# Kernel optimization log

Hardware: AMD Instinct MI355X
Metric: run time of the kernel (lower is better)

The kernel has to match this reference:

```python
import jax, jax.numpy as jnp
import numpy as np

N = 50000      # nodes
E = 800000     # edges (before self-loops)
IN = 128       # input_dim
HID = 64       # hidden_dim
EMB = 32       # embedding_dim
HEADS = 4
NEG_SLOPE = 0.2
BN_EPS = 1e-5


def setup_inputs() -> dict:
    key = jax.random.key(0)
    ks = jax.random.split(key, 20)
    s = 0.1
    x = jax.random.normal(ks[0], (N, IN), jnp.float32)
    edge_index = jax.random.randint(ks[1], (2, E), 0, N, dtype=jnp.int64)
    # GAT layer 0: 128 -> 64, 4 heads, concat
    W0 = jax.random.normal(ks[2], (IN, HEADS * HID), jnp.float32) * s
    a_src0 = jax.random.normal(ks[3], (HEADS, HID), jnp.float32) * s
    a_dst0 = jax.random.normal(ks[4], (HEADS, HID), jnp.float32) * s
    b0 = jax.random.normal(ks[5], (HEADS * HID,), jnp.float32) * s
    # BatchNorm1d(256) in eval mode (running stats)
    bn_gamma = jax.random.uniform(ks[6], (HEADS * HID,), jnp.float32, 0.5, 1.5)
    bn_beta = jax.random.normal(ks[7], (HEADS * HID,), jnp.float32) * s
    bn_mean = jax.random.normal(ks[8], (HEADS * HID,), jnp.float32) * s
    bn_var = jax.random.uniform(ks[9], (HEADS * HID,), jnp.float32, 0.5, 1.5)
    # GAT layer 1: 256 -> 32, 1 head, mean (concat=False)
    W1 = jax.random.normal(ks[10], (HEADS * HID, EMB), jnp.float32) * s
    a_src1 = jax.random.normal(ks[11], (1, EMB), jnp.float32) * s
    a_dst1 = jax.random.normal(ks[12], (1, EMB), jnp.float32) * s
    b1 = jax.random.normal(ks[13], (EMB,), jnp.float32) * s
    # prediction head: Linear(32,64) -> ReLU -> Linear(64,1)
    head_W1 = jax.random.normal(ks[14], (EMB, HID), jnp.float32) * s
    head_b1 = jax.random.normal(ks[15], (HID,), jnp.float32) * s
    head_W2 = jax.random.normal(ks[16], (HID, 1), jnp.float32) * s
    head_b2 = jax.random.normal(ks[17], (1,), jnp.float32) * s
    return dict(x=x, edge_index=edge_index, W0=W0, a_src0=a_src0, a_dst0=a_dst0, b0=b0,
                bn_gamma=bn_gamma, bn_beta=bn_beta, bn_mean=bn_mean, bn_var=bn_var,
                W1=W1, a_src1=a_src1, a_dst1=a_dst1, b1=b1,
                head_W1=head_W1, head_b1=head_b1, head_W2=head_W2, head_b2=head_b2)


def _gat_conv(x, src, dst, W, a_src, a_dst, bias, heads, out_c, concat):
    # PyG GATConv (eval mode, dropout off, self-loops already in src/dst)
    n = x.shape[0]
    h = (x @ W).reshape(n, heads, out_c)                # [N,H,C]
    alpha_s = jnp.sum(h * a_src, axis=-1)               # [N,H]
    alpha_d = jnp.sum(h * a_dst, axis=-1)               # [N,H]
    e = alpha_s[src] + alpha_d[dst]                      # [Etot,H]
    e = jnp.where(e > 0, e, NEG_SLOPE * e)               # leaky_relu
    m = jax.ops.segment_max(e, dst, num_segments=n)      # softmax over incoming edges
    e = jnp.exp(e - m[dst])
    denom = jax.ops.segment_sum(e, dst, num_segments=n)
    alpha = e / denom[dst]                               # [Etot,H]; self-loops ensure denom>0
    out = jax.ops.segment_sum(h[src] * alpha[:, :, None], dst, num_segments=n)  # [N,H,C]
    out = out.reshape(n, heads * out_c) if concat else out.mean(axis=1)
    return out + bias


def reference(x, edge_index, W0, a_src0, a_dst0, b0,
              bn_gamma, bn_beta, bn_mean, bn_var,
              W1, a_src1, a_dst1, b1,
              head_W1, head_b1, head_W2, head_b2):
    n = x.shape[0]
    loops = jnp.arange(n, dtype=edge_index.dtype)
    src = jnp.concatenate([edge_index[0], loops])
    dst = jnp.concatenate([edge_index[1], loops])

    h = _gat_conv(x, src, dst, W0, a_src0, a_dst0, b0, HEADS, HID, True)   # [N,256]
    h = (h - bn_mean) * (bn_gamma / jnp.sqrt(bn_var + BN_EPS)) + bn_beta   # BN eval
    h = jax.nn.relu(h)                                                      # dropout off (eval)
    node_embeddings = _gat_conv(h, src, dst, W1, a_src1, a_dst1, b1, 1, EMB, False)  # [N,32]

    graph_embedding = jnp.mean(node_embeddings, axis=0, keepdims=True)      # [1,32]
    hid = jax.nn.relu(graph_embedding @ head_W1 + head_b1)
    predictions = hid @ head_W2 + head_b2                                    # [1,1]
    return node_embeddings, predictions
```

## Files before the change

kernel.cpp:

```cpp
#include <hip/hip_runtime.h>


#define NEG_SLOPE 0.2f
#define BN_EPS 1e-5f
#define LOG2E 1.4426950408889634f

typedef __attribute__((ext_vector_type(8))) short bf16x8;
typedef __attribute__((ext_vector_type(4))) float f32x4;

__device__ __forceinline__ float bf2f(unsigned short u) {
  return __uint_as_float((unsigned)u << 16);
}
__device__ __forceinline__ unsigned short f2bf(float f) {
  unsigned u = __float_as_uint(f);
  u += 0x7fff + ((u >> 16) & 1);
  return (unsigned short)(u >> 16);
}

__global__ __launch_bounds__(256) void w_swizzle_kernel(
    const float* __restrict__ W0, const float* __restrict__ W1,
    unsigned short* __restrict__ w0sw, unsigned short* __restrict__ w1sw) {
  int o = blockIdx.x * 256 + threadIdx.x;
  if (o < 32768) {
    int j = o & 7, l = (o >> 3) & 63, ks = (o >> 9) & 3,
        ci = (o >> 11) & 3, h = (o >> 13) & 3;
    int row = ks * 32 + (l >> 4) * 8 + j;
    int col = h * 64 + ci * 16 + (l & 15);
    w0sw[o] = f2bf(W0[row * 256 + col]);
  } else if (o < 40960) {
    int o2 = o - 32768;
    int j = o2 & 7, l = (o2 >> 3) & 63, ks = (o2 >> 9) & 7, ci = (o2 >> 12) & 1;
    int row = ks * 32 + (l >> 4) * 8 + j;
    int col = ci * 16 + (l & 15);
    w1sw[o2] = f2bf(W1[row * 32 + col]);
  }
}

__global__ __launch_bounds__(256) void gemm0_mfma_kernel(
    const float* __restrict__ x, const unsigned short* __restrict__ w0sw,
    const float* __restrict__ a_src0, const float* __restrict__ a_dst0,
    unsigned short* __restrict__ h0bf, float* __restrict__ as0,
    float* __restrict__ ad0, int M) {
  __shared__ unsigned short Asw[16 * 64 * 8];
  const int t = threadIdx.x;
  const int lane = t & 63;
  const int h = t >> 6;
  const int row0 = blockIdx.x * 64;

  #pragma unroll
  for (int i = 0; i < 8; ++i) {
    int q = t + 256 * i;
    int r = q >> 5, c4 = q & 31;
    int gr = row0 + r;
    float4 v = make_float4(0.f, 0.f, 0.f, 0.f);
    if (gr < M) v = *reinterpret_cast<const float4*>(&x[(size_t)gr * 128 + c4 * 4]);
    int ks = c4 >> 3;
    int lane_hi = (c4 >> 1) & 3;
    int j0 = (c4 & 1) * 4;
    int slot = (r >> 4) * 4 + ks;
    int dlane = (r & 15) + 16 * lane_hi;
    ushort4 o;
    o.x = f2bf(v.x); o.y = f2bf(v.y); o.z = f2bf(v.z); o.w = f2bf(v.w);
    *reinterpret_cast<ushort4*>(&Asw[(slot * 64 + dlane) * 8 + j0]) = o;
  }
  __syncthreads();

  f32x4 acc[4][4] = {};
  const bf16x8* wp = reinterpret_cast<const bf16x8*>(w0sw);
  #pragma unroll
  for (int ks = 0; ks < 4; ++ks) {
    bf16x8 bfrag[4];
    #pragma unroll
    for (int ci = 0; ci < 4; ++ci)
      bfrag[ci] = wp[(h * 16 + ci * 4 + ks) * 64 + lane];
    #pragma unroll
    for (int ri = 0; ri < 4; ++ri) {
      bf16x8 af = *reinterpret_cast<const bf16x8*>(&Asw[((ri * 4 + ks) * 64 + lane) * 8]);
      #pragma unroll
      for (int ci = 0; ci < 4; ++ci)
        acc[ri][ci] = __builtin_amdgcn_mfma_f32_16x16x32_bf16(af, bfrag[ci], acc[ri][ci], 0, 0, 0);
    }
  }

  float av[4], dv[4];
  #pragma unroll
  for (int ci = 0; ci < 4; ++ci) {
    av[ci] = a_src0[h * 64 + ci * 16 + (lane & 15)];
    dv[ci] = a_dst0[h * 64 + ci * 16 + (lane & 15)];
  }
  const int mrow = (lane >> 4) * 4;
  #pragma unroll
  for (int ri = 0; ri < 4; ++ri) {
    #pragma unroll
    for (int r = 0; r < 4; ++r) {
      int gr = row0 + ri * 16 + mrow + r;
      float ps = acc[ri][0][r] * av[0] + acc[ri][1][r] * av[1] +
                 acc[ri][2][r] * av[2] + acc[ri][3][r] * av[3];
      float pd = acc[ri][0][r] * dv[0] + acc[ri][1][r] * dv[1] +
                 acc[ri][2][r] * dv[2] + acc[ri][3][r] * dv[3];
      #pragma unroll
      for (int off = 1; off < 16; off <<= 1) {
        ps += __shfl_xor(ps, off);
        pd += __shfl_xor(pd, off);
      }
      if (gr < M) {
        #pragma unroll
        for (int ci = 0; ci < 4; ++ci)
          h0bf[(size_t)gr * 256 + h * 64 + ci * 16 + (lane & 15)] = f2bf(acc[ri][ci][r]);
        if ((lane & 15) == 0) { as0[gr * 4 + h] = ps * LOG2E; ad0[gr * 4 + h] = pd * LOG2E; }
      }
    }
  }
}

__global__ __launch_bounds__(256) void gemm1_mfma_kernel(
    const unsigned short* __restrict__ agg0bf,
    const unsigned short* __restrict__ w1sw,
    const float* __restrict__ a_src1, const float* __restrict__ a_dst1,
    unsigned short* __restrict__ h1bf, float* __restrict__ as1,
    float* __restrict__ ad1, int M) {
  const int t = threadIdx.x;
  const int lane = t & 63;
  const int w = t >> 6;
  const int rbase = blockIdx.x * 64 + w * 16;
  const int arow = rbase + (lane & 15);
  const int ar = arow < M ? arow : M - 1;
  const bf16x8* ap = reinterpret_cast<const bf16x8*>(agg0bf) + (size_t)ar * 32;
  const bf16x8* bp = reinterpret_cast<const bf16x8*>(w1sw);

  f32x4 acc[2] = {};
  #pragma unroll
  for (int ks = 0; ks < 8; ++ks) {
    bf16x8 af = ap[ks * 4 + (lane >> 4)];
    acc[0] = __builtin_amdgcn_mfma_f32_16x16x32_bf16(af, bp[(0 * 8 + ks) * 64 + lane], acc[0], 0, 0, 0);
    acc[1] = __builtin_amdgcn_mfma_f32_16x16x32_bf16(af, bp[(1 * 8 + ks) * 64 + lane], acc[1], 0, 0, 0);
  }

  float av[2], dv[2];
  #pragma unroll
  for (int ci = 0; ci < 2; ++ci) {
    av[ci] = a_src1[ci * 16 + (lane & 15)];
    dv[ci] = a_dst1[ci * 16 + (lane & 15)];
  }
  #pragma unroll
  for (int r = 0; r < 4; ++r) {
    int gr = rbase + (lane >> 4) * 4 + r;
    float ps = acc[0][r] * av[0] + acc[1][r] * av[1];
    float pd = acc[0][r] * dv[0] + acc[1][r] * dv[1];
    #pragma unroll
    for (int off = 1; off < 16; off <<= 1) {
      ps += __shfl_xor(ps, off);
      pd += __shfl_xor(pd, off);
    }
    if (gr < M) {
      h1bf[(size_t)gr * 32 + (lane & 15)]      = f2bf(acc[0][r]);
      h1bf[(size_t)gr * 32 + 16 + (lane & 15)] = f2bf(acc[1][r]);
      if ((lane & 15) == 0) { as1[gr] = ps * LOG2E; ad1[gr] = pd * LOG2E; }
    }
  }
}

__global__ __launch_bounds__(256) void hist_kernel(
    const int* __restrict__ dsts, int* __restrict__ deg, int E, int N) {
  int e = blockIdx.x * 256 + threadIdx.x;
  if (e >= E + N) return;
  int d = (e < E) ? dsts[e] : e - E;
  atomicAdd(&deg[d], 1);
}

__global__ __launch_bounds__(256) void scan_block_kernel(
    const int* __restrict__ deg, int* __restrict__ excl,
    int* __restrict__ bsum, int N) {
  __shared__ int tmp[256];
  int i = blockIdx.x * 256 + threadIdx.x;
  int v = (i < N) ? deg[i] : 0;
  tmp[threadIdx.x] = v;
  __syncthreads();
  #pragma unroll
  for (int off = 1; off < 256; off <<= 1) {
    int t = (threadIdx.x >= off) ? tmp[threadIdx.x - off] : 0;
    __syncthreads();
    tmp[threadIdx.x] += t;
    __syncthreads();
  }
  if (i < N) excl[i] = tmp[threadIdx.x] - v;
  if (threadIdx.x == 255) bsum[blockIdx.x] = tmp[255];
}

__global__ __launch_bounds__(256) void scan_add_kernel(
    int* __restrict__ rowptr, const int* __restrict__ bsum,
    int* __restrict__ cursor, int N, int Etot) {
  __shared__ int wred[4];
  const int t = threadIdx.x;
  int v = (t < blockIdx.x) ? bsum[t] : 0;
  #pragma unroll
  for (int off = 32; off >= 1; off >>= 1) v += __shfl_xor(v, off);
  if ((t & 63) == 0) wred[t >> 6] = v;
  __syncthreads();
  const int prefix = wred[0] + wred[1] + wred[2] + wred[3];
  int i = blockIdx.x * 256 + t;
  if (i < N) {
    int r = rowptr[i] + prefix;
    rowptr[i] = r;
    cursor[i] = r;
  }
  if (i == 0) rowptr[N] = Etot;
}

__global__ __launch_bounds__(256) void scatter_kernel(
    const int* __restrict__ srcs, const int* __restrict__ dsts,
    int* __restrict__ cursor, int* __restrict__ csr_src, int E, int N) {
  int e = blockIdx.x * 256 + threadIdx.x;
  if (e >= E + N) return;
  int s, d;
  if (e < E) { s = srcs[e]; d = dsts[e]; } else { s = d = e - E; }
  int pos = atomicAdd(&cursor[d], 1);
  csr_src[pos] = s;
}

__global__ __launch_bounds__(256) void agg0_kernel(
    const int* __restrict__ rowptr, const int* __restrict__ csr_src,
    const unsigned short* __restrict__ h0bf, const float* __restrict__ as0,
    const float* __restrict__ ad0, const float* __restrict__ b0,
    const float* __restrict__ gamma, const float* __restrict__ beta,
    const float* __restrict__ mean, const float* __restrict__ var,
    unsigned short* __restrict__ outbf, int N) {
  __shared__ float wlds[4][64];
  const int lane = threadIdx.x & 63;
  const int wid = threadIdx.x >> 6;
  const int n = blockIdx.x * 4 + wid;
  if (n >= N) return;
  const int h = lane >> 4;
  const int eidx = lane & 15;
  const int bb = lane & 48;
  const int beg = rowptr[n], end = rowptr[n + 1];
  const float adv = ad0[n * 4 + h];
  float4 acc = make_float4(0.f, 0.f, 0.f, 0.f);
  float wsum = 0.f;

  for (int i = beg; i < end; i += 16) {
    const int rem = end - i;
    const int ne = rem < 16 ? rem : 16;
    const int li = (eidx < ne) ? eidx : (ne - 1);
    const int src = csr_src[i + li];
    float xx = as0[(unsigned)(src * 4 + h)] + adv;
    xx = fmaxf(xx, NEG_SLOPE * xx);
    float wl = (eidx < ne) ? exp2f(xx) : 0.f;
    wsum += wl;
    wlds[wid][lane] = wl;
    int e = 0;
    for (; e + 8 <= ne; e += 8) {
      const int s0 = __builtin_amdgcn_readlane(src, e + 0);
      const int s1 = __builtin_amdgcn_readlane(src, e + 1);
      const int s2 = __builtin_amdgcn_readlane(src, e + 2);
      const int s3 = __builtin_amdgcn_readlane(src, e + 3);
      const int s4 = __builtin_amdgcn_readlane(src, e + 4);
      const int s5 = __builtin_amdgcn_readlane(src, e + 5);
      const int s6 = __builtin_amdgcn_readlane(src, e + 6);
      const int s7 = __builtin_amdgcn_readlane(src, e + 7);
      ushort4 v0 = *reinterpret_cast<const ushort4*>(&(h0bf + (size_t)s0 * 256)[lane * 4]);
      ushort4 v1 = *reinterpret_cast<const ushort4*>(&(h0bf + (size_t)s1 * 256)[lane * 4]);
      ushort4 v2 = *reinterpret_cast<const ushort4*>(&(h0bf + (size_t)s2 * 256)[lane * 4]);
      ushort4 v3 = *reinterpret_cast<const ushort4*>(&(h0bf + (size_t)s3 * 256)[lane * 4]);
      ushort4 v4 = *reinterpret_cast<const ushort4*>(&(h0bf + (size_t)s4 * 256)[lane * 4]);
      ushort4 v5 = *reinterpret_cast<const ushort4*>(&(h0bf + (size_t)s5 * 256)[lane * 4]);
      ushort4 v6 = *reinterpret_cast<const ushort4*>(&(h0bf + (size_t)s6 * 256)[lane * 4]);
      ushort4 v7 = *reinterpret_cast<const ushort4*>(&(h0bf + (size_t)s7 * 256)[lane * 4]);
      const float w0 = wlds[wid][bb + e + 0];
      const float w1 = wlds[wid][bb + e + 1];
      const float w2 = wlds[wid][bb + e + 2];
      const float w3 = wlds[wid][bb + e + 3];
      const float w4 = wlds[wid][bb + e + 4];
      const float w5 = wlds[wid][bb + e + 5];
      const float w6 = wlds[wid][bb + e + 6];
      const float w7 = wlds[wid][bb + e + 7];
      acc.x += ((w0 * bf2f(v0.x) + w1 * bf2f(v1.x)) + (w2 * bf2f(v2.x) + w3 * bf2f(v3.x))) +
               ((w4 * bf2f(v4.x) + w5 * bf2f(v5.x)) + (w6 * bf2f(v6.x) + w7 * bf2f(v7.x)));
      acc.y += ((w0 * bf2f(v0.y) + w1 * bf2f(v1.y)) + (w2 * bf2f(v2.y) + w3 * bf2f(v3.y))) +
               ((w4 * bf2f(v4.y) + w5 * bf2f(v5.y)) + (w6 * bf2f(v6.y) + w7 * bf2f(v7.y)));
      acc.z += ((w0 * bf2f(v0.z) + w1 * bf2f(v1.z)) + (w2 * bf2f(v2.z) + w3 * bf2f(v3.z))) +
               ((w4 * bf2f(v4.z) + w5 * bf2f(v5.z)) + (w6 * bf2f(v6.z) + w7 * bf2f(v7.z)));
      acc.w += ((w0 * bf2f(v0.w) + w1 * bf2f(v1.w)) + (w2 * bf2f(v2.w) + w3 * bf2f(v3.w))) +
               ((w4 * bf2f(v4.w) + w5 * bf2f(v5.w)) + (w6 * bf2f(v6.w) + w7 * bf2f(v7.w)));
    }
    for (; e < ne; ++e) {
      const int s0 = __builtin_amdgcn_readlane(src, e);
      const float w0 = wlds[wid][bb + e];
      ushort4 v = *reinterpret_cast<const ushort4*>(&(h0bf + (size_t)s0 * 256)[lane * 4]);
      acc.x += w0 * bf2f(v.x); acc.y += w0 * bf2f(v.y);
      acc.z += w0 * bf2f(v.z); acc.w += w0 * bf2f(v.w);
    }
  }

  #pragma unroll
  for (int off = 1; off < 16; off <<= 1) wsum += __shfl_xor(wsum, off);

  float inv = 1.0f / wsum;
  int j = lane * 4;
  float4 bbv = *reinterpret_cast<const float4*>(&b0[j]);
  float4 mu = *reinterpret_cast<const float4*>(&mean[j]);
  float4 gg = *reinterpret_cast<const float4*>(&gamma[j]);
  float4 vv = *reinterpret_cast<const float4*>(&var[j]);
  float4 be = *reinterpret_cast<const float4*>(&beta[j]);
  float4 o;
  o.x = (acc.x * inv + bbv.x - mu.x) * (gg.x * rsqrtf(vv.x + BN_EPS)) + be.x;
  o.y = (acc.y * inv + bbv.y - mu.y) * (gg.y * rsqrtf(vv.y + BN_EPS)) + be.y;
  o.z = (acc.z * inv + bbv.z - mu.z) * (gg.z * rsqrtf(vv.z + BN_EPS)) + be.z;
  o.w = (acc.w * inv + bbv.w - mu.w) * (gg.w * rsqrtf(vv.w + BN_EPS)) + be.w;
  ushort4 ob;
  ob.x = f2bf(fmaxf(o.x, 0.f)); ob.y = f2bf(fmaxf(o.y, 0.f));
  ob.z = f2bf(fmaxf(o.z, 0.f)); ob.w = f2bf(fmaxf(o.w, 0.f));
  *reinterpret_cast<ushort4*>(&outbf[(size_t)n * 256 + j]) = ob;
}

__global__ __launch_bounds__(256) void agg1_kernel(
    const int* __restrict__ rowptr, const int* __restrict__ csr_src,
    const unsigned short* __restrict__ h1bf, const float* __restrict__ as1,
    const float* __restrict__ ad1, const float* __restrict__ b1,
    float* __restrict__ out, int N) {
  const int t = threadIdx.x;
  const int lane = t & 63;
  const int w = t >> 6;
  const int n = blockIdx.x * 4 + w;
  if (n >= N) return;
  const int c = lane & 31;
  const int half = lane >> 5;
  const int beg = rowptr[n], end = rowptr[n + 1];
  const float adv = ad1[n];
  float acc = 0.f, wsum = 0.f;
  int i = beg + half;
  for (; i + 6 < end; i += 8) {
    int s0 = csr_src[i + 0], s1 = csr_src[i + 2],
        s2 = csr_src[i + 4], s3 = csr_src[i + 6];
    float x0 = as1[s0] + adv, x1 = as1[s1] + adv,
          x2 = as1[s2] + adv, x3 = as1[s3] + adv;
    unsigned short u0 = h1bf[(size_t)s0 * 32 + c];
    unsigned short u1 = h1bf[(size_t)s1 * 32 + c];
    unsigned short u2 = h1bf[(size_t)s2 * 32 + c];
    unsigned short u3 = h1bf[(size_t)s3 * 32 + c];
    float w0 = exp2f(fmaxf(x0, NEG_SLOPE * x0)),
          w1 = exp2f(fmaxf(x1, NEG_SLOPE * x1)),
          w2 = exp2f(fmaxf(x2, NEG_SLOPE * x2)),
          w3 = exp2f(fmaxf(x3, NEG_SLOPE * x3));
    wsum += (w0 + w1) + (w2 + w3);
    acc += w0 * bf2f(u0) + w1 * bf2f(u1) + w2 * bf2f(u2) + w3 * bf2f(u3);
  }
  for (; i < end; i += 2) {
    int s = csr_src[i];
    float xx = as1[s] + adv;
    float wgt = exp2f(fmaxf(xx, NEG_SLOPE * xx));
    wsum += wgt;
    acc += wgt * bf2f(h1bf[(size_t)s * 32 + c]);
  }
  acc += __shfl_xor(acc, 32);
  wsum += __shfl_xor(wsum, 32);
  if (half == 0) out[(size_t)n * 32 + c] = acc / wsum + b1[c];
}

__global__ __launch_bounds__(256) void gsum_kernel(
    const float* __restrict__ out, float* __restrict__ gsum,
    int* __restrict__ ticket,
    const float* __restrict__ hW1, const float* __restrict__ hb1,
    const float* __restrict__ hW2, const float* __restrict__ hb2,
    float* __restrict__ pout, int N) {
  __shared__ float red[8][32];
  __shared__ int lastblk;
  const int t = threadIdx.x;
  const int c = t & 31;
  float s = 0.f;
  const size_t total = (size_t)N * 32;
  for (size_t j = (size_t)blockIdx.x * 256 + t; j < total;
       j += (size_t)gridDim.x * 256)
    s += out[j];
  red[t >> 5][c] = s;
  __syncthreads();
  if (t < 32) {
    float v = 0.f;
    #pragma unroll
    for (int i = 0; i < 8; ++i) v += red[i][t];
    atomicAdd(&gsum[t], v);
  }
  __threadfence();
  if (t == 0) {
    int old = __hip_atomic_fetch_add(ticket, 1, __ATOMIC_ACQ_REL,
                                     __HIP_MEMORY_SCOPE_AGENT);
    lastblk = (old == (int)gridDim.x - 1);
  }
  __syncthreads();
  if (lastblk && t < 64) {
    float invN = 1.0f / (float)N;
    float acc = hb1[t];
    #pragma unroll
    for (int cc = 0; cc < 32; ++cc) {
      float gv = __hip_atomic_load(&gsum[cc], __ATOMIC_RELAXED,
                                   __HIP_MEMORY_SCOPE_AGENT);
      acc += (gv * invN) * hW1[cc * 64 + t];
    }
    acc = fmaxf(acc, 0.f);
    float v = acc * hW2[t];
    #pragma unroll
    for (int off = 1; off < 64; off <<= 1) v += __shfl_xor(v, off);
    if (t == 0) pout[(size_t)N * 32] = v + hb2[0];
  }
}

extern "C" void kernel_launch(void* const* d_in, const int* in_sizes, int n_in,
                              void* d_out, int out_size, void* d_ws, size_t ws_size,
                              hipStream_t stream) {
  const float* x       = (const float*)d_in[0];
  const int*   ei      = (const int*)d_in[1];
  const float* W0      = (const float*)d_in[2];
  const float* a_src0  = (const float*)d_in[3];
  const float* a_dst0  = (const float*)d_in[4];
  const float* b0      = (const float*)d_in[5];
  const float* bn_g    = (const float*)d_in[6];
  const float* bn_b    = (const float*)d_in[7];
  const float* bn_m    = (const float*)d_in[8];
  const float* bn_v    = (const float*)d_in[9];
  const float* W1      = (const float*)d_in[10];
  const float* a_src1  = (const float*)d_in[11];
  const float* a_dst1  = (const float*)d_in[12];
  const float* b1      = (const float*)d_in[13];
  const float* hW1     = (const float*)d_in[14];
  const float* hb1     = (const float*)d_in[15];
  const float* hW2     = (const float*)d_in[16];
  const float* hb2     = (const float*)d_in[17];

  const int N = in_sizes[0] / 128;
  const int E = in_sizes[1] / 2;
  const int Etot = E + N;
  const int* srcs = ei;
  const int* dsts = ei + E;
  const int NB = (N + 255) / 256;

  float* out = (float*)d_out;

  float* ws = (float*)d_ws;
  size_t off = 0;
  unsigned short* h0bf   = (unsigned short*)(ws + off); off += (size_t)N * 128;
  unsigned short* agg0bf = (unsigned short*)(ws + off); off += (size_t)N * 128;
  unsigned short* h1bf   = (unsigned short*)(ws + off); off += (size_t)N * 16;
  unsigned short* w0sw   = (unsigned short*)(ws + off); off += 16384;
  unsigned short* w1sw   = (unsigned short*)(ws + off); off += 4096;
  float* as0    = ws + off; off += (size_t)N * 4;
  float* ad0    = ws + off; off += (size_t)N * 4;
  float* as1    = ws + off; off += (size_t)N;
  float* ad1    = ws + off; off += (size_t)N;
  int* rowptr   = (int*)(ws + off); off += (size_t)N + 1;
  int* cursor   = (int*)(ws + off); off += (size_t)N;
  int* bsum     = (int*)(ws + off); off += 256;
  int* csr_src  = (int*)(ws + off); off += (size_t)Etot;
  size_t zoff = off;
  int* deg      = (int*)(ws + off); off += (size_t)N;
  float* gsum   = ws + off; off += 32;
  int* ticket   = (int*)(ws + off); off += 1;

  hipMemsetAsync(ws + zoff, 0, (off - zoff) * sizeof(float), stream);

  auto cdiv = [](long a, long b) { return (int)((a + b - 1) / b); };

  hist_kernel<<<cdiv(Etot, 256), 256, 0, stream>>>(dsts, deg, E, N);
  scan_block_kernel<<<NB, 256, 0, stream>>>(deg, rowptr, bsum, N);
  scan_add_kernel<<<NB, 256, 0, stream>>>(rowptr, bsum, cursor, N, Etot);
  scatter_kernel<<<cdiv(Etot, 256), 256, 0, stream>>>(srcs, dsts, cursor, csr_src, E, N);

  w_swizzle_kernel<<<160, 256, 0, stream>>>(W0, W1, w0sw, w1sw);

  gemm0_mfma_kernel<<<cdiv(N, 64), 256, 0, stream>>>(
      x, w0sw, a_src0, a_dst0, h0bf, as0, ad0, N);
  agg0_kernel<<<cdiv(N, 4), 256, 0, stream>>>(rowptr, csr_src, h0bf, as0, ad0,
                                              b0, bn_g, bn_b, bn_m, bn_v, agg0bf, N);

  gemm1_mfma_kernel<<<cdiv(N, 64), 256, 0, stream>>>(
      agg0bf, w1sw, a_src1, a_dst1, h1bf, as1, ad1, N);
  agg1_kernel<<<cdiv(N, 4), 256, 0, stream>>>(rowptr, csr_src, h1bf, as1, ad1,
                                              b1, out, N);

  gsum_kernel<<<128, 256, 0, stream>>>(out, gsum, ticket, hW1, hb1, hW2, hb2, out, N);
}
```

Before: 258.8 us.

## Split agg0 into column slices per block with head-major attention scores

Attention score arrays as0/ad0 are stored head-major so each head's scores are contiguous. agg0 now assigns each block one of 8 column slices of 32 features (one half of a head) and processes nodes in a grid-stride loop over 2048 node-blocks. Within a wave, 8 edges are gathered in parallel, each by 8 lanes reading 8 bytes, and the partial sums are reduced with cross-lane shuffles. The LDS weight staging is dropped. The aim is to improve L2 locality by having concurrent blocks touch only a narrow slice of h0bf. The cost is that the CSR indices and scores are reread 8 times, and each gather is a small segment per row.

```diff
diff --git a/kernel.cpp b/kernel.cpp
--- a/kernel.cpp
+++ b/kernel.cpp
@@ -107,7 +107,10 @@
         #pragma unroll
         for (int ci = 0; ci < 4; ++ci)
           h0bf[(size_t)gr * 256 + h * 64 + ci * 16 + (lane & 15)] = f2bf(acc[ri][ci][r]);
-        if ((lane & 15) == 0) { as0[gr * 4 + h] = ps * LOG2E; ad0[gr * 4 + h] = pd * LOG2E; }
+        if ((lane & 15) == 0) {
+          as0[(size_t)h * M + gr] = ps * LOG2E;
+          ad0[(size_t)h * M + gr] = pd * LOG2E;
+        }
       }
     }
   }
@@ -224,93 +227,66 @@
     const float* __restrict__ ad0, const float* __restrict__ b0,
     const float* __restrict__ gamma, const float* __restrict__ beta,
     const float* __restrict__ mean, const float* __restrict__ var,
-    unsigned short* __restrict__ outbf, int N) {
-  __shared__ float wlds[4][64];
+    unsigned short* __restrict__ outbf, int N, int nodeStride) {
   const int lane = threadIdx.x & 63;
   const int wid = threadIdx.x >> 6;
-  const int n = blockIdx.x * 4 + wid;
-  if (n >= N) return;
-  const int h = lane >> 4;
-  const int eidx = lane & 15;
-  const int bb = lane & 48;
-  const int beg = rowptr[n], end = rowptr[n + 1];
-  const float adv = ad0[n * 4 + h];
-  float4 acc = make_float4(0.f, 0.f, 0.f, 0.f);
-  float wsum = 0.f;
-
-  for (int i = beg; i < end; i += 16) {
-    const int rem = end - i;
-    const int ne = rem < 16 ? rem : 16;
-    const int li = (eidx < ne) ? eidx : (ne - 1);
-    const int src = csr_src[i + li];
-    float xx = as0[(unsigned)(src * 4 + h)] + adv;
-    xx = fmaxf(xx, NEG_SLOPE * xx);
-    float wl = (eidx < ne) ? exp2f(xx) : 0.f;
-    wsum += wl;
-    wlds[wid][lane] = wl;
-    int e = 0;
-    for (; e + 8 <= ne; e += 8) {
-      const int s0 = __builtin_amdgcn_readlane(src, e + 0);
-      const int s1 = __builtin_amdgcn_readlane(src, e + 1);
-      const int s2 = __builtin_amdgcn_readlane(src, e + 2);
-      const int s3 = __builtin_amdgcn_readlane(src, e + 3);
-      const int s4 = __builtin_amdgcn_readlane(src, e + 4);
-      const int s5 = __builtin_amdgcn_readlane(src, e + 5);
-      const int s6 = __builtin_amdgcn_readlane(src, e + 6);
-      const int s7 = __builtin_amdgcn_readlane(src, e + 7);
-      ushort4 v0 = *reinterpret_cast<const ushort4*>(&(h0bf + (size_t)s0 * 256)[lane * 4]);
-      ushort4 v1 = *reinterpret_cast<const ushort4*>(&(h0bf + (size_t)s1 * 256)[lane * 4]);
-      ushort4 v2 = *reinterpret_cast<const ushort4*>(&(h0bf + (size_t)s2 * 256)[lane * 4]);
-      ushort4 v3 = *reinterpret_cast<const ushort4*>(&(h0bf + (size_t)s3 * 256)[lane * 4]);
-      ushort4 v4 = *reinterpret_cast<const ushort4*>(&(h0bf + (size_t)s4 * 256)[lane * 4]);
-      ushort4 v5 = *reinterpret_cast<const ushort4*>(&(h0bf + (size_t)s5 * 256)[lane * 4]);
-      ushort4 v6 = *reinterpret_cast<const ushort4*>(&(h0bf + (size_t)s6 * 256)[lane * 4]);
-      ushort4 v7 = *reinterpret_cast<const ushort4*>(&(h0bf + (size_t)s7 * 256)[lane * 4]);
-      const float w0 = wlds[wid][bb + e + 0];
-      const float w1 = wlds[wid][bb + e + 1];
-      const float w2 = wlds[wid][bb + e + 2];
-      const float w3 = wlds[wid][bb + e + 3];
-      const float w4 = wlds[wid][bb + e + 4];
-      const float w5 = wlds[wid][bb + e + 5];
-      const float w6 = wlds[wid][bb + e + 6];
-      const float w7 = wlds[wid][bb + e + 7];
-      acc.x += ((w0 * bf2f(v0.x) + w1 * bf2f(v1.x)) + (w2 * bf2f(v2.x) + w3 * bf2f(v3.x))) +
-               ((w4 * bf2f(v4.x) + w5 * bf2f(v5.x)) + (w6 * bf2f(v6.x) + w7 * bf2f(v7.x)));
-      acc.y += ((w0 * bf2f(v0.y) + w1 * bf2f(v1.y)) + (w2 * bf2f(v2.y) + w3 * bf2f(v3.y))) +
-               ((w4 * bf2f(v4.y) + w5 * bf2f(v5.y)) + (w6 * bf2f(v6.y) + w7 * bf2f(v7.y)));
-      acc.z += ((w0 * bf2f(v0.z) + w1 * bf2f(v1.z)) + (w2 * bf2f(v2.z) + w3 * bf2f(v3.z))) +
-               ((w4 * bf2f(v4.z) + w5 * bf2f(v5.z)) + (w6 * bf2f(v6.z) + w7 * bf2f(v7.z)));
-      acc.w += ((w0 * bf2f(v0.w) + w1 * bf2f(v1.w)) + (w2 * bf2f(v2.w) + w3 * bf2f(v3.w))) +
-               ((w4 * bf2f(v4.w) + w5 * bf2f(v5.w)) + (w6 * bf2f(v6.w) + w7 * bf2f(v7.w)));
-    }
-    for (; e < ne; ++e) {
-      const int s0 = __builtin_amdgcn_readlane(src, e);
-      const float w0 = wlds[wid][bb + e];
-      ushort4 v = *reinterpret_cast<const ushort4*>(&(h0bf + (size_t)s0 * 256)[lane * 4]);
-      acc.x += w0 * bf2f(v.x); acc.y += w0 * bf2f(v.y);
-      acc.z += w0 * bf2f(v.z); acc.w += w0 * bf2f(v.w);
-    }
-  }
-
-  #pragma unroll
-  for (int off = 1; off < 16; off <<= 1) wsum += __shfl_xor(wsum, off);
-
-  float inv = 1.0f / wsum;
-  int j = lane * 4;
-  float4 bbv = *reinterpret_cast<const float4*>(&b0[j]);
-  float4 mu = *reinterpret_cast<const float4*>(&mean[j]);
-  float4 gg = *reinterpret_cast<const float4*>(&gamma[j]);
-  float4 vv = *reinterpret_cast<const float4*>(&var[j]);
-  float4 be = *reinterpret_cast<const float4*>(&beta[j]);
-  float4 o;
-  o.x = (acc.x * inv + bbv.x - mu.x) * (gg.x * rsqrtf(vv.x + BN_EPS)) + be.x;
-  o.y = (acc.y * inv + bbv.y - mu.y) * (gg.y * rsqrtf(vv.y + BN_EPS)) + be.y;
-  o.z = (acc.z * inv + bbv.z - mu.z) * (gg.z * rsqrtf(vv.z + BN_EPS)) + be.z;
-  o.w = (acc.w * inv + bbv.w - mu.w) * (gg.w * rsqrtf(vv.w + BN_EPS)) + be.w;
-  ushort4 ob;
-  ob.x = f2bf(fmaxf(o.x, 0.f)); ob.y = f2bf(fmaxf(o.y, 0.f));
-  ob.z = f2bf(fmaxf(o.z, 0.f)); ob.w = f2bf(fmaxf(o.w, 0.f));
-  *reinterpret_cast<ushort4*>(&outbf[(size_t)n * 256 + j]) = ob;
+  const int s = blockIdx.x & 7;
+  const int h = s >> 1;
+  const int e8 = lane >> 3;
+  const int l = lane & 7;
+  const unsigned colw = (unsigned)(s * 32 + l * 4);
+  const float* __restrict__ as0h = as0 + (size_t)h * N;
+  const float* __restrict__ ad0h = ad0 + (size_t)h * N;
+
+  for (int n = (blockIdx.x >> 3) * 4 + wid; n < N; n += nodeStride) {
+    const int beg = rowptr[n], end = rowptr[n + 1];
+    const float adv = ad0h[n];
+    float4 acc = make_float4(0.f, 0.f, 0.f, 0.f);
+    float wsum = 0.f;
+    for (int i = beg; i < end; i += 16) {
+      int ne = end - i; if (ne > 16) ne = 16;
+      const int ia = e8, ib = e8 + 8;
+      const int sa = __builtin_nontemporal_load(&csr_src[i + (ia < ne ? ia : ne - 1)]);
+      const int sb = __builtin_nontemporal_load(&csr_src[i + (ib < ne ? ib : ne - 1)]);
+      const float xa = as0h[sa] + adv;
+      const float xb = as0h[sb] + adv;
+      const ushort4 va = *reinterpret_cast<const ushort4*>(&h0bf[((unsigned)sa << 8) + colw]);
+      const ushort4 vb = *reinterpret_cast<const ushort4*>(&h0bf[((unsigned)sb << 8) + colw]);
+      const float wa = (ia < ne) ? exp2f(fmaxf(xa, NEG_SLOPE * xa)) : 0.f;
+      const float wb = (ib < ne) ? exp2f(fmaxf(xb, NEG_SLOPE * xb)) : 0.f;
+      wsum += wa + wb;
+      acc.x += wa * bf2f(va.x) + wb * bf2f(vb.x);
+      acc.y += wa * bf2f(va.y) + wb * bf2f(vb.y);
+      acc.z += wa * bf2f(va.z) + wb * bf2f(vb.z);
+      acc.w += wa * bf2f(va.w) + wb * bf2f(vb.w);
+    }
+    #pragma unroll
+    for (int off = 8; off < 64; off <<= 1) {
+      acc.x += __shfl_xor(acc.x, off);
+      acc.y += __shfl_xor(acc.y, off);
+      acc.z += __shfl_xor(acc.z, off);
+      acc.w += __shfl_xor(acc.w, off);
+      wsum  += __shfl_xor(wsum, off);
+    }
+    if (e8 == 0) {
+      const float inv = 1.0f / wsum;
+      const int j = (int)colw;
+      float4 bbv = *reinterpret_cast<const float4*>(&b0[j]);
+      float4 mu = *reinterpret_cast<const float4*>(&mean[j]);
+      float4 gg = *reinterpret_cast<const float4*>(&gamma[j]);
+      float4 vv = *reinterpret_cast<const float4*>(&var[j]);
+      float4 be = *reinterpret_cast<const float4*>(&beta[j]);
+      float4 o;
+      o.x = (acc.x * inv + bbv.x - mu.x) * (gg.x * rsqrtf(vv.x + BN_EPS)) + be.x;
+      o.y = (acc.y * inv + bbv.y - mu.y) * (gg.y * rsqrtf(vv.y + BN_EPS)) + be.y;
+      o.z = (acc.z * inv + bbv.z - mu.z) * (gg.z * rsqrtf(vv.z + BN_EPS)) + be.z;
+      o.w = (acc.w * inv + bbv.w - mu.w) * (gg.w * rsqrtf(vv.w + BN_EPS)) + be.w;
+      ushort4 ob;
+      ob.x = f2bf(fmaxf(o.x, 0.f)); ob.y = f2bf(fmaxf(o.y, 0.f));
+      ob.z = f2bf(fmaxf(o.z, 0.f)); ob.w = f2bf(fmaxf(o.w, 0.f));
+      *reinterpret_cast<ushort4*>(&outbf[(size_t)n * 256 + colw]) = ob;
+    }
+  }
 }
 
 __global__ __launch_bounds__(256) void agg1_kernel(
@@ -468,8 +444,10 @@
 
   gemm0_mfma_kernel<<<cdiv(N, 64), 256, 0, stream>>>(
       x, w0sw, a_src0, a_dst0, h0bf, as0, ad0, N);
-  agg0_kernel<<<cdiv(N, 4), 256, 0, stream>>>(rowptr, csr_src, h0bf, as0, ad0,
-                                              b0, bn_g, bn_b, bn_m, bn_v, agg0bf, N);
+  const int NODE_BLOCKS = 2048;
+  agg0_kernel<<<8 * NODE_BLOCKS, 256, 0, stream>>>(
+      rowptr, csr_src, h0bf, as0, ad0, b0, bn_g, bn_b, bn_m, bn_v,
+      agg0bf, N, NODE_BLOCKS * 4);
 
   gemm1_mfma_kernel<<<cdiv(N, 64), 256, 0, stream>>>(
       agg0bf, w1sw, a_src1, a_dst1, h1bf, as1, ad1, N);
```

Measured after the change: 386.6 us. 49.4% more time.

## Fuse layer-1 GEMM into agg0 epilogue and stage agg1 edge weights in LDS

Applied to the files above, without the earlier changes.

The agg0 kernel now writes its BN+ReLU output for 4 nodes into a swizzled LDS tile, and one wave runs the 256->32 MFMA GEMM with attention logits directly. This removes the agg0bf intermediate (N*256 bf16 written and reread) and the separate gemm1 launch. In exchange the MFMA runs on a 16-row tile with only 4 valid rows, and each block pays a __syncthreads. agg1 also computes edge weights once per 16-edge chunk into LDS instead of each half-wave recomputing exp for its own edges.

```diff
diff --git a/kernel.cpp b/kernel.cpp
--- a/kernel.cpp
+++ b/kernel.cpp
@@ -113,53 +113,6 @@
   }
 }
 
-__global__ __launch_bounds__(256) void gemm1_mfma_kernel(
-    const unsigned short* __restrict__ agg0bf,
-    const unsigned short* __restrict__ w1sw,
-    const float* __restrict__ a_src1, const float* __restrict__ a_dst1,
-    unsigned short* __restrict__ h1bf, float* __restrict__ as1,
-    float* __restrict__ ad1, int M) {
-  const int t = threadIdx.x;
-  const int lane = t & 63;
-  const int w = t >> 6;
-  const int rbase = blockIdx.x * 64 + w * 16;
-  const int arow = rbase + (lane & 15);
-  const int ar = arow < M ? arow : M - 1;
-  const bf16x8* ap = reinterpret_cast<const bf16x8*>(agg0bf) + (size_t)ar * 32;
-  const bf16x8* bp = reinterpret_cast<const bf16x8*>(w1sw);
-
-  f32x4 acc[2] = {};
-  #pragma unroll
-  for (int ks = 0; ks < 8; ++ks) {
-    bf16x8 af = ap[ks * 4 + (lane >> 4)];
-    acc[0] = __builtin_amdgcn_mfma_f32_16x16x32_bf16(af, bp[(0 * 8 + ks) * 64 + lane], acc[0], 0, 0, 0);
-    acc[1] = __builtin_amdgcn_mfma_f32_16x16x32_bf16(af, bp[(1 * 8 + ks) * 64 + lane], acc[1], 0, 0, 0);
-  }
-
-  float av[2], dv[2];
-  #pragma unroll
-  for (int ci = 0; ci < 2; ++ci) {
-    av[ci] = a_src1[ci * 16 + (lane & 15)];
-    dv[ci] = a_dst1[ci * 16 + (lane & 15)];
-  }
-  #pragma unroll
-  for (int r = 0; r < 4; ++r) {
-    int gr = rbase + (lane >> 4) * 4 + r;
-    float ps = acc[0][r] * av[0] + acc[1][r] * av[1];
-    float pd = acc[0][r] * dv[0] + acc[1][r] * dv[1];
-    #pragma unroll
-    for (int off = 1; off < 16; off <<= 1) {
-      ps += __shfl_xor(ps, off);
-      pd += __shfl_xor(pd, off);
-    }
-    if (gr < M) {
-      h1bf[(size_t)gr * 32 + (lane & 15)]      = f2bf(acc[0][r]);
-      h1bf[(size_t)gr * 32 + 16 + (lane & 15)] = f2bf(acc[1][r]);
-      if ((lane & 15) == 0) { as1[gr] = ps * LOG2E; ad1[gr] = pd * LOG2E; }
-    }
-  }
-}
-
 __global__ __launch_bounds__(256) void hist_kernel(
     const int* __restrict__ dsts, int* __restrict__ deg, int E, int N) {
   int e = blockIdx.x * 256 + threadIdx.x;
@@ -224,93 +177,135 @@
     const float* __restrict__ ad0, const float* __restrict__ b0,
     const float* __restrict__ gamma, const float* __restrict__ beta,
     const float* __restrict__ mean, const float* __restrict__ var,
-    unsigned short* __restrict__ outbf, int N) {
+    const unsigned short* __restrict__ w1sw,
+    const float* __restrict__ a_src1, const float* __restrict__ a_dst1,
+    unsigned short* __restrict__ h1bf, float* __restrict__ as1,
+    float* __restrict__ ad1, int N) {
   __shared__ float wlds[4][64];
+  __shared__ unsigned short Asw2[8 * 64 * 8];
   const int lane = threadIdx.x & 63;
   const int wid = threadIdx.x >> 6;
   const int n = blockIdx.x * 4 + wid;
-  if (n >= N) return;
+  const bool valid = n < N;
   const int h = lane >> 4;
   const int eidx = lane & 15;
   const int bb = lane & 48;
-  const int beg = rowptr[n], end = rowptr[n + 1];
-  const float adv = ad0[n * 4 + h];
-  float4 acc = make_float4(0.f, 0.f, 0.f, 0.f);
-  float wsum = 0.f;
-
-  for (int i = beg; i < end; i += 16) {
-    const int rem = end - i;
-    const int ne = rem < 16 ? rem : 16;
-    const int li = (eidx < ne) ? eidx : (ne - 1);
-    const int src = csr_src[i + li];
-    float xx = as0[(unsigned)(src * 4 + h)] + adv;
-    xx = fmaxf(xx, NEG_SLOPE * xx);
-    float wl = (eidx < ne) ? exp2f(xx) : 0.f;
-    wsum += wl;
-    wlds[wid][lane] = wl;
-    int e = 0;
-    for (; e + 8 <= ne; e += 8) {
-      const int s0 = __builtin_amdgcn_readlane(src, e + 0);
-      const int s1 = __builtin_amdgcn_readlane(src, e + 1);
-      const int s2 = __builtin_amdgcn_readlane(src, e + 2);
-      const int s3 = __builtin_amdgcn_readlane(src, e + 3);
-      const int s4 = __builtin_amdgcn_readlane(src, e + 4);
-      const int s5 = __builtin_amdgcn_readlane(src, e + 5);
-      const int s6 = __builtin_amdgcn_readlane(src, e + 6);
-      const int s7 = __builtin_amdgcn_readlane(src, e + 7);
-      ushort4 v0 = *reinterpret_cast<const ushort4*>(&(h0bf + (size_t)s0 * 256)[lane * 4]);
-      ushort4 v1 = *reinterpret_cast<const ushort4*>(&(h0bf + (size_t)s1 * 256)[lane * 4]);
-      ushort4 v2 = *reinterpret_cast<const ushort4*>(&(h0bf + (size_t)s2 * 256)[lane * 4]);
-      ushort4 v3 = *reinterpret_cast<const ushort4*>(&(h0bf + (size_t)s3 * 256)[lane * 4]);
-      ushort4 v4 = *reinterpret_cast<const ushort4*>(&(h0bf + (size_t)s4 * 256)[lane * 4]);
-      ushort4 v5 = *reinterpret_cast<const ushort4*>(&(h0bf + (size_t)s5 * 256)[lane * 4]);
-      ushort4 v6 = *reinterpret_cast<const ushort4*>(&(h0bf + (size_t)s6 * 256)[lane * 4]);
-      ushort4 v7 = *reinterpret_cast<const ushort4*>(&(h0bf + (size_t)s7 * 256)[lane * 4]);
-      const float w0 = wlds[wid][bb + e + 0];
-      const float w1 = wlds[wid][bb + e + 1];
-      const float w2 = wlds[wid][bb + e + 2];
-      const float w3 = wlds[wid][bb + e + 3];
-      const float w4 = wlds[wid][bb + e + 4];
-      const float w5 = wlds[wid][bb + e + 5];
-      const float w6 = wlds[wid][bb + e + 6];
-      const float w7 = wlds[wid][bb + e + 7];
-      acc.x += ((w0 * bf2f(v0.x) + w1 * bf2f(v1.x)) + (w2 * bf2f(v2.x) + w3 * bf2f(v3.x))) +
-               ((w4 * bf2f(v4.x) + w5 * bf2f(v5.x)) + (w6 * bf2f(v6.x) + w7 * bf2f(v7.x)));
-      acc.y += ((w0 * bf2f(v0.y) + w1 * bf2f(v1.y)) + (w2 * bf2f(v2.y) + w3 * bf2f(v3.y))) +
-               ((w4 * bf2f(v4.y) + w5 * bf2f(v5.y)) + (w6 * bf2f(v6.y) + w7 * bf2f(v7.y)));
-      acc.z += ((w0 * bf2f(v0.z) + w1 * bf2f(v1.z)) + (w2 * bf2f(v2.z) + w3 * bf2f(v3.z))) +
-               ((w4 * bf2f(v4.z) + w5 * bf2f(v5.z)) + (w6 * bf2f(v6.z) + w7 * bf2f(v7.z)));
-      acc.w += ((w0 * bf2f(v0.w) + w1 * bf2f(v1.w)) + (w2 * bf2f(v2.w) + w3 * bf2f(v3.w))) +
-               ((w4 * bf2f(v4.w) + w5 * bf2f(v5.w)) + (w6 * bf2f(v6.w) + w7 * bf2f(v7.w)));
-    }
-    for (; e < ne; ++e) {
-      const int s0 = __builtin_amdgcn_readlane(src, e);
-      const float w0 = wlds[wid][bb + e];
-      ushort4 v = *reinterpret_cast<const ushort4*>(&(h0bf + (size_t)s0 * 256)[lane * 4]);
-      acc.x += w0 * bf2f(v.x); acc.y += w0 * bf2f(v.y);
-      acc.z += w0 * bf2f(v.z); acc.w += w0 * bf2f(v.w);
-    }
-  }
-
-  #pragma unroll
-  for (int off = 1; off < 16; off <<= 1) wsum += __shfl_xor(wsum, off);
-
-  float inv = 1.0f / wsum;
-  int j = lane * 4;
-  float4 bbv = *reinterpret_cast<const float4*>(&b0[j]);
-  float4 mu = *reinterpret_cast<const float4*>(&mean[j]);
-  float4 gg = *reinterpret_cast<const float4*>(&gamma[j]);
-  float4 vv = *reinterpret_cast<const float4*>(&var[j]);
-  float4 be = *reinterpret_cast<const float4*>(&beta[j]);
-  float4 o;
-  o.x = (acc.x * inv + bbv.x - mu.x) * (gg.x * rsqrtf(vv.x + BN_EPS)) + be.x;
-  o.y = (acc.y * inv + bbv.y - mu.y) * (gg.y * rsqrtf(vv.y + BN_EPS)) + be.y;
-  o.z = (acc.z * inv + bbv.z - mu.z) * (gg.z * rsqrtf(vv.z + BN_EPS)) + be.z;
-  o.w = (acc.w * inv + bbv.w - mu.w) * (gg.w * rsqrtf(vv.w + BN_EPS)) + be.w;
-  ushort4 ob;
-  ob.x = f2bf(fmaxf(o.x, 0.f)); ob.y = f2bf(fmaxf(o.y, 0.f));
-  ob.z = f2bf(fmaxf(o.z, 0.f)); ob.w = f2bf(fmaxf(o.w, 0.f));
-  *reinterpret_cast<ushort4*>(&outbf[(size_t)n * 256 + j]) = ob;
+
+  if (valid) {
+    const int beg = rowptr[n], end = rowptr[n + 1];
+    const float adv = ad0[n * 4 + h];
+    float4 acc = make_float4(0.f, 0.f, 0.f, 0.f);
+    float wsum = 0.f;
+
+    for (int i = beg; i < end; i += 16) {
+      const int rem = end - i;
+      const int ne = rem < 16 ? rem : 16;
+      const int li = (eidx < ne) ? eidx : (ne - 1);
+      const int src = csr_src[i + li];
+      float xx = as0[(unsigned)(src * 4 + h)] + adv;
+      xx = fmaxf(xx, NEG_SLOPE * xx);
+      float wl = (eidx < ne) ? exp2f(xx) : 0.f;
+      wsum += wl;
+      wlds[wid][lane] = wl;
+      int e = 0;
+      for (; e + 8 <= ne; e += 8) {
+        const int s0 = __builtin_amdgcn_readlane(src, e + 0);
+        const int s1 = __builtin_amdgcn_readlane(src, e + 1);
+        const int s2 = __builtin_amdgcn_readlane(src, e + 2);
+        const int s3 = __builtin_amdgcn_readlane(src, e + 3);
+        const int s4 = __builtin_amdgcn_readlane(src, e + 4);
+        const int s5 = __builtin_amdgcn_readlane(src, e + 5);
+        const int s6 = __builtin_amdgcn_readlane(src, e + 6);
+        const int s7 = __builtin_amdgcn_readlane(src, e + 7);
+        ushort4 v0 = *reinterpret_cast<const ushort4*>(&(h0bf + (size_t)s0 * 256)[lane * 4]);
+        ushort4 v1 = *reinterpret_cast<const ushort4*>(&(h0bf + (size_t)s1 * 256)[lane * 4]);
+        ushort4 v2 = *reinterpret_cast<const ushort4*>(&(h0bf + (size_t)s2 * 256)[lane * 4]);
+        ushort4 v3 = *reinterpret_cast<const ushort4*>(&(h0bf + (size_t)s3 * 256)[lane * 4]);
+        ushort4 v4 = *reinterpret_cast<const ushort4*>(&(h0bf + (size_t)s4 * 256)[lane * 4]);
+        ushort4 v5 = *reinterpret_cast<const ushort4*>(&(h0bf + (size_t)s5 * 256)[lane * 4]);
+        ushort4 v6 = *reinterpret_cast<const ushort4*>(&(h0bf + (size_t)s6 * 256)[lane * 4]);
+        ushort4 v7 = *reinterpret_cast<const ushort4*>(&(h0bf + (size_t)s7 * 256)[lane * 4]);
+        const float w0 = wlds[wid][bb + e + 0];
+        const float w1 = wlds[wid][bb + e + 1];
+        const float w2 = wlds[wid][bb + e + 2];
+        const float w3 = wlds[wid][bb + e + 3];
+        const float w4 = wlds[wid][bb + e + 4];
+        const float w5 = wlds[wid][bb + e + 5];
+        const float w6 = wlds[wid][bb + e + 6];
+        const float w7 = wlds[wid][bb + e + 7];
+        acc.x += ((w0 * bf2f(v0.x) + w1 * bf2f(v1.x)) + (w2 * bf2f(v2.x) + w3 * bf2f(v3.x))) +
+                 ((w4 * bf2f(v4.x) + w5 * bf2f(v5.x)) + (w6 * bf2f(v6.x) + w7 * bf2f(v7.x)));
+        acc.y += ((w0 * bf2f(v0.y) + w1 * bf2f(v1.y)) + (w2 * bf2f(v2.y) + w3 * bf2f(v3.y))) +
+                 ((w4 * bf2f(v4.y) + w5 * bf2f(v5.y)) + (w6 * bf2f(v6.y) + w7 * bf2f(v7.y)));
+        acc.z += ((w0 * bf2f(v0.z) + w1 * bf2f(v1.z)) + (w2 * bf2f(v2.z) + w3 * bf2f(v3.z))) +
+                 ((w4 * bf2f(v4.z) + w5 * bf2f(v5.z)) + (w6 * bf2f(v6.z) + w7 * bf2f(v7.z)));
+        acc.w += ((w0 * bf2f(v0.w) + w1 * bf2f(v1.w)) + (w2 * bf2f(v2.w) + w3 * bf2f(v3.w))) +
+                 ((w4 * bf2f(v4.w) + w5 * bf2f(v5.w)) + (w6 * bf2f(v6.w) + w7 * bf2f(v7.w)));
+      }
+      for (; e < ne; ++e) {
+        const int s0 = __builtin_amdgcn_readlane(src, e);
+        const float w0 = wlds[wid][bb + e];
+        ushort4 v = *reinterpret_cast<const ushort4*>(&(h0bf + (size_t)s0 * 256)[lane * 4]);
+        acc.x += w0 * bf2f(v.x); acc.y += w0 * bf2f(v.y);
+        acc.z += w0 * bf2f(v.z); acc.w += w0 * bf2f(v.w);
+      }
+    }
+
+    #pragma unroll
+    for (int off = 1; off < 16; off <<= 1) wsum += __shfl_xor(wsum, off);
+
+    const float inv = 1.0f / wsum;
+    const int j = lane * 4;
+    float4 bbv = *reinterpret_cast<const float4*>(&b0[j]);
+    float4 mu = *reinterpret_cast<const float4*>(&mean[j]);
+    float4 gg = *reinterpret_cast<const float4*>(&gamma[j]);
+    float4 vv = *reinterpret_cast<const float4*>(&var[j]);
+    float4 be = *reinterpret_cast<const float4*>(&beta[j]);
+    float4 o;
+    o.x = (acc.x * inv + bbv.x - mu.x) * (gg.x * rsqrtf(vv.x + BN_EPS)) + be.x;
+    o.y = (acc.y * inv + bbv.y - mu.y) * (gg.y * rsqrtf(vv.y + BN_EPS)) + be.y;
+    o.z = (acc.z * inv + bbv.z - mu.z) * (gg.z * rsqrtf(vv.z + BN_EPS)) + be.z;
+    o.w = (acc.w * inv + bbv.w - mu.w) * (gg.w * rsqrtf(vv.w + BN_EPS)) + be.w;
+    ushort4 ob;
+    ob.x = f2bf(fmaxf(o.x, 0.f)); ob.y = f2bf(fmaxf(o.y, 0.f));
+    ob.z = f2bf(fmaxf(o.z, 0.f)); ob.w = f2bf(fmaxf(o.w, 0.f));
+    const int ks = lane >> 3;
+    const int lane_hi = (lane >> 1) & 3;
+    const int j0 = (lane & 1) * 4;
+    const int dlane = wid + 16 * lane_hi;
+    *reinterpret_cast<ushort4*>(&Asw2[(ks * 64 + dlane) * 8 + j0]) = ob;
+  }
+  __syncthreads();
+
+  if (wid == 0) {
+    const bf16x8* bp = reinterpret_cast<const bf16x8*>(w1sw);
+    f32x4 c0 = {}, c1 = {};
+    #pragma unroll
+    for (int ks = 0; ks < 8; ++ks) {
+      bf16x8 af = *reinterpret_cast<const bf16x8*>(&Asw2[(ks * 64 + lane) * 8]);
+      c0 = __builtin_amdgcn_mfma_f32_16x16x32_bf16(af, bp[(0 * 8 + ks) * 64 + lane], c0, 0, 0, 0);
+      c1 = __builtin_amdgcn_mfma_f32_16x16x32_bf16(af, bp[(1 * 8 + ks) * 64 + lane], c1, 0, 0, 0);
+    }
+    const float av0 = a_src1[lane & 15], av1 = a_src1[16 + (lane & 15)];
+    const float dv0 = a_dst1[lane & 15], dv1 = a_dst1[16 + (lane & 15)];
+    const int rowgrp = lane >> 4;
+    #pragma unroll
+    for (int r = 0; r < 4; ++r) {
+      float ps = c0[r] * av0 + c1[r] * av1;
+      float pd = c0[r] * dv0 + c1[r] * dv1;
+      #pragma unroll
+      for (int off = 1; off < 16; off <<= 1) {
+        ps += __shfl_xor(ps, off);
+        pd += __shfl_xor(pd, off);
+      }
+      const int gn = blockIdx.x * 4 + r;
+      if (rowgrp == 0 && gn < N) {
+        h1bf[(size_t)gn * 32 + (lane & 15)]      = f2bf(c0[r]);
+        h1bf[(size_t)gn * 32 + 16 + (lane & 15)] = f2bf(c1[r]);
+        if ((lane & 15) == 0) { as1[gn] = ps * LOG2E; ad1[gn] = pd * LOG2E; }
+      }
+    }
+  }
 }
 
 __global__ __launch_bounds__(256) void agg1_kernel(
@@ -318,42 +313,47 @@
     const unsigned short* __restrict__ h1bf, const float* __restrict__ as1,
     const float* __restrict__ ad1, const float* __restrict__ b1,
     float* __restrict__ out, int N) {
+  __shared__ float wslab[4][16];
+  __shared__ int sslab[4][16];
   const int t = threadIdx.x;
   const int lane = t & 63;
-  const int w = t >> 6;
-  const int n = blockIdx.x * 4 + w;
+  const int wid = t >> 6;
+  const int n = blockIdx.x * 4 + wid;
   if (n >= N) return;
   const int c = lane & 31;
   const int half = lane >> 5;
   const int beg = rowptr[n], end = rowptr[n + 1];
   const float adv = ad1[n];
   float acc = 0.f, wsum = 0.f;
-  int i = beg + half;
-  for (; i + 6 < end; i += 8) {
-    int s0 = csr_src[i + 0], s1 = csr_src[i + 2],
-        s2 = csr_src[i + 4], s3 = csr_src[i + 6];
-    float x0 = as1[s0] + adv, x1 = as1[s1] + adv,
-          x2 = as1[s2] + adv, x3 = as1[s3] + adv;
-    unsigned short u0 = h1bf[(size_t)s0 * 32 + c];
-    unsigned short u1 = h1bf[(size_t)s1 * 32 + c];
-    unsigned short u2 = h1bf[(size_t)s2 * 32 + c];
-    unsigned short u3 = h1bf[(size_t)s3 * 32 + c];
-    float w0 = exp2f(fmaxf(x0, NEG_SLOPE * x0)),
-          w1 = exp2f(fmaxf(x1, NEG_SLOPE * x1)),
-          w2 = exp2f(fmaxf(x2, NEG_SLOPE * x2)),
-          w3 = exp2f(fmaxf(x3, NEG_SLOPE * x3));
-    wsum += (w0 + w1) + (w2 + w3);
-    acc += w0 * bf2f(u0) + w1 * bf2f(u1) + w2 * bf2f(u2) + w3 * bf2f(u3);
-  }
-  for (; i < end; i += 2) {
-    int s = csr_src[i];
-    float xx = as1[s] + adv;
-    float wgt = exp2f(fmaxf(xx, NEG_SLOPE * xx));
-    wsum += wgt;
-    acc += wgt * bf2f(h1bf[(size_t)s * 32 + c]);
-  }
+
+  for (int i = beg; i < end; i += 16) {
+    int ne = end - i; if (ne > 16) ne = 16;
+    if (lane < 16) {
+      const int idx = lane < ne ? lane : ne - 1;
+      const int s = csr_src[i + idx];
+      const float x = as1[s] + adv;
+      const float wl = (lane < ne) ? exp2f(fmaxf(x, NEG_SLOPE * x)) : 0.f;
+      wslab[wid][lane] = wl;
+      sslab[wid][lane] = s;
+      wsum += wl;
+    }
+    for (int e = 0; e < ne; e += 8) {
+      const int i0 = e + half, i1 = e + 2 + half, i2 = e + 4 + half, i3 = e + 6 + half;
+      const int s0 = sslab[wid][i0], s1 = sslab[wid][i1],
+                s2 = sslab[wid][i2], s3 = sslab[wid][i3];
+      const float w0 = wslab[wid][i0], w1 = wslab[wid][i1],
+                  w2 = wslab[wid][i2], w3 = wslab[wid][i3];
+      const unsigned short u0 = h1bf[(size_t)s0 * 32 + c];
+      const unsigned short u1 = h1bf[(size_t)s1 * 32 + c];
+      const unsigned short u2 = h1bf[(size_t)s2 * 32 + c];
+      const unsigned short u3 = h1bf[(size_t)s3 * 32 + c];
+      acc += (w0 * bf2f(u0) + w1 * bf2f(u1)) + (w2 * bf2f(u2) + w3 * bf2f(u3));
+    }
+  }
+  #pragma unroll
+  for (int off = 1; off < 16; off <<= 1) wsum += __shfl_xor(wsum, off);
+  wsum = __shfl(wsum, lane & 15);
   acc += __shfl_xor(acc, 32);
-  wsum += __shfl_xor(wsum, 32);
   if (half == 0) out[(size_t)n * 32 + c] = acc / wsum + b1[c];
 }
 
@@ -438,7 +438,6 @@
   float* ws = (float*)d_ws;
   size_t off = 0;
   unsigned short* h0bf   = (unsigned short*)(ws + off); off += (size_t)N * 128;
-  unsigned short* agg0bf = (unsigned short*)(ws + off); off += (size_t)N * 128;
   unsigned short* h1bf   = (unsigned short*)(ws + off); off += (size_t)N * 16;
   unsigned short* w0sw   = (unsigned short*)(ws + off); off += 16384;
   unsigned short* w1sw   = (unsigned short*)(ws + off); off += 4096;
@@ -468,11 +467,10 @@
 
   gemm0_mfma_kernel<<<cdiv(N, 64), 256, 0, stream>>>(
       x, w0sw, a_src0, a_dst0, h0bf, as0, ad0, N);
-  agg0_kernel<<<cdiv(N, 4), 256, 0, stream>>>(rowptr, csr_src, h0bf, as0, ad0,
-                                              b0, bn_g, bn_b, bn_m, bn_v, agg0bf, N);
-
-  gemm1_mfma_kernel<<<cdiv(N, 64), 256, 0, stream>>>(
-      agg0bf, w1sw, a_src1, a_dst1, h1bf, as1, ad1, N);
+  agg0_kernel<<<cdiv(N, 4), 256, 0, stream>>>(
+      rowptr, csr_src, h0bf, as0, ad0, b0, bn_g, bn_b, bn_m, bn_v,
+      w1sw, a_src1, a_dst1, h1bf, as1, ad1, N);
+
   agg1_kernel<<<cdiv(N, 4), 256, 0, stream>>>(rowptr, csr_src, h1bf, as1, ad1,
                                               b1, out, N);
 
```

Result: faster. 251.3 us (-2.9%).
